# Kernel optimization log

Hardware: AMD Instinct MI355X
Metric: run time of the kernel (lower is better)

The kernel has to match this reference:

```python
import jax, jax.numpy as jnp
import numpy as np

B, S, D, QD, OUT = 32, 2048, 768, 256, 1024

def setup_inputs() -> dict:
    key = jax.random.key(0)
    k = jax.random.split(key, 8)
    data = jax.random.normal(k[0], (B, S, D), dtype=jnp.float32)
    seq_len = jax.random.randint(k[1], (B,), 0, S)
    # learned params (Linear: y = x @ W.T + b)
    s1 = 1.0 / np.sqrt(D)
    s3 = 1.0 / np.sqrt(QD)
    W1 = jax.random.uniform(k[2], (QD, D), minval=-s1, maxval=s1, dtype=jnp.float32)
    b1 = jax.random.uniform(k[3], (QD,), minval=-s1, maxval=s1, dtype=jnp.float32)
    W2 = jax.random.uniform(k[4], (QD, D), minval=-s1, maxval=s1, dtype=jnp.float32)
    b2 = jax.random.uniform(k[5], (QD,), minval=-s1, maxval=s1, dtype=jnp.float32)
    W3 = jax.random.uniform(k[6], (OUT, QD), minval=-s3, maxval=s3, dtype=jnp.float32)
    b3 = jax.random.uniform(k[7], (OUT,), minval=-s3, maxval=s3, dtype=jnp.float32)
    return {"data": data, "seq_len": seq_len, "W1": W1, "b1": b1,
            "W2": W2, "b2": b2, "W3": W3, "b3": b3}

def reference(data, seq_len, W1, b1, W2, b2, W3, b3):
    # Q, K projections: [B,S,QD]
    Q = jnp.einsum('bsd,qd->bsq', data, W1) + b1
    K = jnp.einsum('bsd,qd->bsq', data, W2) + b2
    # scores = K @ Q^T / sqrt(QD): [B,S,S]
    scores = jnp.einsum('biq,bjq->bij', K, Q) / np.sqrt(QD).astype(np.float32)
    attn = jax.nn.softmax(scores, axis=2)
    # attention output uses K as values: [B,S,QD]
    x = jnp.einsum('bij,bjq->biq', attn, K)
    # max-pool over sequence dim -> [B,QD]
    x = jnp.max(x, axis=1)
    out = jax.nn.relu(jnp.einsum('bq,oq->bo', x, W3) + b3)
    return out
```

## Files before the change

kernel.cpp:

```cpp
#include <hip/hip_runtime.h>
#include <hip/hip_bf16.h>

#define Bn   32
#define Sn   2048
#define Dn   768
#define QDn  256
#define OUTn 1024

typedef __attribute__((ext_vector_type(8))) short          bf16x8;
typedef __attribute__((ext_vector_type(4))) float          f32x4;
typedef __attribute__((ext_vector_type(8))) unsigned short u16x8;
typedef __attribute__((ext_vector_type(4))) unsigned short u16x4;

typedef unsigned short ushort_t;

__device__ __forceinline__ unsigned short f2bf(float f) {
    unsigned int u = __float_as_uint(f);
    u = (u + 0x7FFFu + ((u >> 16) & 1u)) >> 16;
    return (unsigned short)u;
}
#define MFMA16(a,b,c) __builtin_amdgcn_mfma_f32_16x16x32_bf16((a),(b),(c),0,0,0)

__global__ __launch_bounds__(256) void wconv_kernel(
    const float* __restrict__ W1, const float* __restrict__ W2,
    ushort_t* __restrict__ W1h, ushort_t* __restrict__ W2h)
{
    const int idx = blockIdx.x * 256 + threadIdx.x;
    W1h[idx] = f2bf(W1[idx]);
    W2h[idx] = f2bf(W2[idx]);
}

__global__ __launch_bounds__(256, 2) void proj_kernel(
    const float* __restrict__ data,
    const ushort_t* __restrict__ W1h, const float* __restrict__ b1,
    const ushort_t* __restrict__ W2h, const float* __restrict__ b2,
    ushort_t* __restrict__ Qb, ushort_t* __restrict__ Kb,
    ushort_t* __restrict__ KTb)
{
    __shared__ __align__(16) char smem[34816];
    ushort_t* DH = (ushort_t*)smem;
    ushort_t* WH = (ushort_t*)(smem + 10240);
    ushort_t* EP = (ushort_t*)smem;

    const int tid  = threadIdx.x;
    const int w    = tid >> 6;
    const int quad = (tid >> 4) & 3;
    const int n15  = tid & 15;
    const int mtile = blockIdx.y;
    const int half  = blockIdx.x;
    const bool isQ  = (half == 0);
    const ushort_t* WhP = isQ ? W1h : W2h;
    const float* bp = isQ ? b1 : b2;

    f32x4 acc[2][16];
    #pragma unroll
    for (int i = 0; i < 2; ++i)
        #pragma unroll
        for (int j = 0; j < 16; ++j) acc[i][j] = (f32x4)0.f;

    const size_t drow = (size_t)mtile * 128;

    for (int kt = 0; kt < 24; ++kt) {
        const int kc = kt * 32;
        {
            const int m  = tid >> 1;
            const int k0 = (tid & 1) << 4;
            const float* src = data + (drow + m) * 768 + kc + k0;
            const float4 v0 = *(const float4*)(src);
            const float4 v1 = *(const float4*)(src + 4);
            const float4 v2 = *(const float4*)(src + 8);
            const float4 v3 = *(const float4*)(src + 12);
            u16x8 h0, h1;
            h0[0]=f2bf(v0.x); h0[1]=f2bf(v0.y); h0[2]=f2bf(v0.z); h0[3]=f2bf(v0.w);
            h0[4]=f2bf(v1.x); h0[5]=f2bf(v1.y); h0[6]=f2bf(v1.z); h0[7]=f2bf(v1.w);
            h1[0]=f2bf(v2.x); h1[1]=f2bf(v2.y); h1[2]=f2bf(v2.z); h1[3]=f2bf(v2.w);
            h1[4]=f2bf(v3.x); h1[5]=f2bf(v3.y); h1[6]=f2bf(v3.z); h1[7]=f2bf(v3.w);
            *(u16x8*)&DH[m*40 + k0]     = h0;
            *(u16x8*)&DH[m*40 + k0 + 8] = h1;
        }
        #pragma unroll
        for (int u = 0; u < 4; ++u) {
            const int nrow = (tid >> 2) + u * 64;
            const int ko   = (tid & 3) << 3;
            *(u16x8*)&WH[nrow*40 + ko] = *(const u16x8*)(WhP + (size_t)nrow * 768 + kc + ko);
        }
        __syncthreads();
        bf16x8 ah[2];
        #pragma unroll
        for (int ms = 0; ms < 2; ++ms)
            ah[ms] = *(bf16x8*)&DH[(w*32 + ms*16 + n15)*40 + quad*8];
        #pragma unroll
        for (int ns = 0; ns < 16; ++ns) {
            const bf16x8 bh = *(bf16x8*)&WH[(ns*16 + n15)*40 + quad*8];
            #pragma unroll
            for (int ms = 0; ms < 2; ++ms)
                acc[ms][ns] = MFMA16(ah[ms], bh, acc[ms][ns]);
        }
        __syncthreads();
    }

    float bv[16];
    #pragma unroll
    for (int ns = 0; ns < 16; ++ns) bv[ns] = bp[ns*16 + n15];

    {
        ushort_t* dstRM = isQ ? Qb : Kb;
        #pragma unroll
        for (int hf = 0; hf < 2; ++hf) {
            __syncthreads();
            if ((w >> 1) == hf) {
                #pragma unroll
                for (int ms = 0; ms < 2; ++ms)
                    #pragma unroll
                    for (int ns = 0; ns < 16; ++ns)
                        #pragma unroll
                        for (int r = 0; r < 4; ++r) {
                            const int rl = (w & 1)*32 + ms*16 + quad*4 + r;
                            EP[rl*264 + ns*16 + n15] = f2bf(acc[ms][ns][r] + bv[ns]);
                        }
            }
            __syncthreads();
            const int row = tid >> 2;
            #pragma unroll
            for (int u = 0; u < 8; ++u) {
                const int co = (tid & 3)*8 + u*32;
                *(u16x8*)(dstRM + (drow + hf*64 + row)*256 + co) =
                    *(u16x8*)&EP[row*264 + co];
            }
        }
    }
    if (!isQ) {
        const int bidx = mtile >> 4;
        const int s0   = (mtile & 15) * 128;
        #pragma unroll
        for (int qh = 0; qh < 2; ++qh) {
            __syncthreads();
            #pragma unroll
            for (int ms = 0; ms < 2; ++ms)
                #pragma unroll
                for (int ns8 = 0; ns8 < 8; ++ns8) {
                    const int ns = qh*8 + ns8;
                    #pragma unroll
                    for (int r = 0; r < 4; ++r) {
                        const int rowm = w*32 + ms*16 + quad*4 + r;
                        EP[(ns8*16 + n15)*136 + rowm] = f2bf(acc[ms][ns][r] + bv[ns]);
                    }
                }
            __syncthreads();
            const int q = tid >> 1;
            #pragma unroll
            for (int u = 0; u < 8; ++u) {
                const int mo = (tid & 1)*8 + u*16;
                *(u16x8*)(KTb + ((size_t)(bidx*256 + qh*128 + q))*2048 + s0 + mo) =
                    *(u16x8*)&EP[q*136 + mo];
            }
        }
    }
}

__global__ __launch_bounds__(256, 2) void attn_kernel(
    const ushort_t* __restrict__ Qb, const ushort_t* __restrict__ Kb,
    const ushort_t* __restrict__ KTb, float* __restrict__ pmax)
{
    __shared__ __align__(16) char smem[49664];
    ushort_t* QS = (ushort_t*)smem;
    ushort_t* PS = (ushort_t*)(smem + 32768);
    float*    l_lds = (float*)(smem + 49152);

    const int tid  = threadIdx.x;
    const int w    = tid >> 6;
    const int quad = (tid >> 4) & 3;
    const int n15  = tid & 15;
    const int b    = blockIdx.x;
    const int it   = blockIdx.y;
    const int i0   = it * 128;

    const ushort_t* QbB  = Qb  + (size_t)b * Sn * QDn;
    const ushort_t* KbB  = Kb  + (size_t)b * Sn * QDn;
    const ushort_t* KTbB = KTb + (size_t)b * QDn * Sn;

    bf16x8 kf[2][8];
    #pragma unroll
    for (int isub = 0; isub < 2; ++isub) {
        const size_t irow = (size_t)(i0 + w*32 + isub*16 + n15) * QDn;
        #pragma unroll
        for (int ks = 0; ks < 8; ++ks)
            kf[isub][ks] = *(const bf16x8*)(KbB + irow + ks*32 + quad*8);
    }

    f32x4 xq[4][8];
    #pragma unroll
    for (int qs = 0; qs < 4; ++qs)
        #pragma unroll
        for (int is = 0; is < 8; ++is) xq[qs][is] = (f32x4)0.f;
    float l_i[2] = {0.f, 0.f};

    const int swz  = (n15 & 7) * 8;
    const int jrow = tid >> 2;
    const int wsw  = (jrow & 7) * 8;

    for (int jt = 0; jt < Sn; jt += 64) {
        __syncthreads();
        {
            const ushort_t* src = QbB + (size_t)(jt + jrow) * QDn + (tid & 3) * 64;
            ushort_t* dst = QS + jrow * 256;
            #pragma unroll
            for (int u = 0; u < 8; ++u) {
                const int col = (tid & 3) * 64 + u * 8;
                *(u16x8*)&dst[col ^ wsw] = *(const u16x8*)(src + u * 8);
            }
        }
        __syncthreads();
        f32x4 sc[4][2];
        #pragma unroll
        for (int js = 0; js < 4; ++js) { sc[js][0] = (f32x4)0.f; sc[js][1] = (f32x4)0.f; }
        #pragma unroll
        for (int ks = 0; ks < 8; ++ks) {
            #pragma unroll
            for (int js = 0; js < 4; ++js) {
                const bf16x8 ah = *(bf16x8*)&QS[(js*16 + n15)*256 + ((ks*32 + quad*8) ^ swz)];
                sc[js][0] = MFMA16(ah, kf[0][ks], sc[js][0]);
                sc[js][1] = MFMA16(ah, kf[1][ks], sc[js][1]);
            }
        }
        #pragma unroll
        for (int isub = 0; isub < 2; ++isub) {
            const int prow = (w*32 + isub*16 + n15) * 64;
            float rs = 0.f;
            #pragma unroll
            for (int js = 0; js < 4; ++js) {
                u16x4 ph;
                #pragma unroll
                for (int r = 0; r < 4; ++r) {
                    const float p = __expf(sc[js][isub][r] * 0.0625f);
                    rs += p;
                    ph[r] = f2bf(p);
                }
                *(u16x4*)&PS[prow + ((js*16 + quad*4) ^ swz)] = ph;
            }
            rs += __shfl_xor(rs, 16, 64);
            rs += __shfl_xor(rs, 32, 64);
            l_i[isub] += rs;
        }
        bf16x8 at2[2][4];
        #pragma unroll
        for (int ks2 = 0; ks2 < 2; ++ks2)
            #pragma unroll
            for (int qs = 0; qs < 4; ++qs)
                at2[ks2][qs] = *(const bf16x8*)(
                    KTbB + (size_t)(w*64 + qs*16 + n15) * Sn + jt + ks2*32 + quad*8);
        __syncthreads();
        #pragma unroll
        for (int ks2 = 0; ks2 < 2; ++ks2) {
            #pragma unroll
            for (int is = 0; is < 8; ++is) {
                const bf16x8 pb = *(bf16x8*)&PS[(is*16 + n15)*64 + ((ks2*32 + quad*8) ^ swz)];
                #pragma unroll
                for (int qs = 0; qs < 4; ++qs)
                    xq[qs][is] = MFMA16(at2[ks2][qs], pb, xq[qs][is]);
            }
        }
    }

    __syncthreads();
    if (quad == 0) {
        l_lds[w*32 + n15]      = l_i[0];
        l_lds[w*32 + 16 + n15] = l_i[1];
    }
    __syncthreads();
    float linv[8];
    #pragma unroll
    for (int is = 0; is < 8; ++is) linv[is] = 1.0f / l_lds[is*16 + n15];
    #pragma unroll
    for (int qs = 0; qs < 4; ++qs) {
        #pragma unroll
        for (int r = 0; r < 4; ++r) {
            float mv = xq[qs][0][r] * linv[0];
            #pragma unroll
            for (int is = 1; is < 8; ++is)
                mv = fmaxf(mv, xq[qs][is][r] * linv[is]);
            mv = fmaxf(mv, __shfl_xor(mv, 1, 64));
            mv = fmaxf(mv, __shfl_xor(mv, 2, 64));
            mv = fmaxf(mv, __shfl_xor(mv, 4, 64));
            mv = fmaxf(mv, __shfl_xor(mv, 8, 64));
            if (n15 == 0) {
                const int q = w*64 + qs*16 + quad*4 + r;
                pmax[((size_t)b * 16 + it) * QDn + q] = mv;
            }
        }
    }
}

__global__ __launch_bounds__(256) void head_kernel(
    const float* __restrict__ pmax,
    const float* __restrict__ W3, const float* __restrict__ b3,
    float* __restrict__ out)
{
    __shared__ float xs[QDn];
    const int b = blockIdx.x, tid = threadIdx.x;
    float m = pmax[((size_t)b * 16) * QDn + tid];
    #pragma unroll
    for (int t = 1; t < 16; ++t)
        m = fmaxf(m, pmax[((size_t)b * 16 + t) * QDn + tid]);
    xs[tid] = m;
    __syncthreads();
    #pragma unroll
    for (int u = 0; u < 4; ++u) {
        const int o = (u << 8) + tid;
        const float4* wv = (const float4*)(W3 + (size_t)o * QDn);
        float s = 0.f;
        #pragma unroll 8
        for (int q4 = 0; q4 < QDn / 4; ++q4) {
            const float4 w4 = wv[q4];
            const float4 x4 = *(const float4*)&xs[q4 << 2];
            s += w4.x * x4.x + w4.y * x4.y + w4.z * x4.z + w4.w * x4.w;
        }
        out[(size_t)b * OUTn + o] = fmaxf(s + b3[o], 0.f);
    }
}

extern "C" void kernel_launch(void* const* d_in, const int* in_sizes, int n_in,
                              void* d_out, int out_size, void* d_ws, size_t ws_size,
                              hipStream_t stream) {
    const float* data = (const float*)d_in[0];
    const float* W1 = (const float*)d_in[2];
    const float* b1 = (const float*)d_in[3];
    const float* W2 = (const float*)d_in[4];
    const float* b2 = (const float*)d_in[5];
    const float* W3 = (const float*)d_in[6];
    const float* b3 = (const float*)d_in[7];
    float* out = (float*)d_out;

    ushort_t* Qb  = (ushort_t*)d_ws;
    ushort_t* Kb  = Qb  + 16777216;
    ushort_t* KTb = Kb  + 16777216;
    float*    pmax = (float*)((char*)d_ws + 100663296);
    ushort_t* W1h = (ushort_t*)((char*)d_ws + 100663296 + 524288);
    ushort_t* W2h = W1h + 196608;

    wconv_kernel<<<768, 256, 0, stream>>>(W1, W2, W1h, W2h);
    dim3 gP(2, 512);
    proj_kernel<<<gP, 256, 0, stream>>>(data, W1h, b1, W2h, b2, Qb, Kb, KTb);
    dim3 gA(Bn, 16);
    attn_kernel<<<gA, 256, 0, stream>>>(Qb, Kb, KTb, pmax);
    head_kernel<<<Bn, 256, 0, stream>>>(pmax, W3, b3, out);
}
```

Baseline: 663.9 us.

## Async global-to-LDS Q loads, pre-convert data to bf16, split head kernel

The attention kernel now stages each Q tile into LDS with global_load_lds instructions issued for the next tile while the current PV MFMAs run. This replaces the synchronous register round-trip and drops one barrier per iteration. The KT loads are also issued earlier. When the workspace is large enough, a separate kernel converts data to bf16 first so the projection kernel reads half the bytes, at the cost of an extra pass over the input. The head kernel is split across four blocks per batch to add parallelism.

```diff
diff --git a/kernel.cpp b/kernel.cpp
--- a/kernel.cpp
+++ b/kernel.cpp
@@ -21,6 +21,13 @@
 }
 #define MFMA16(a,b,c) __builtin_amdgcn_mfma_f32_16x16x32_bf16((a),(b),(c),0,0,0)
 
+__device__ __forceinline__ void gll16(const ushort_t* g, ushort_t* l) {
+    __builtin_amdgcn_global_load_lds(
+        (const __attribute__((address_space(1))) unsigned int*)g,
+        (__attribute__((address_space(3))) unsigned int*)l,
+        16, 0, 0);
+}
+
 __global__ __launch_bounds__(256) void wconv_kernel(
     const float* __restrict__ W1, const float* __restrict__ W2,
     ushort_t* __restrict__ W1h, ushort_t* __restrict__ W2h)
@@ -30,8 +37,21 @@
     W2h[idx] = f2bf(W2[idx]);
 }
 
+__global__ __launch_bounds__(256) void dconv_kernel(
+    const float* __restrict__ in, ushort_t* __restrict__ outb)
+{
+    const size_t i8 = ((size_t)blockIdx.x * 256 + threadIdx.x) * 8;
+    const float4 a = *(const float4*)(in + i8);
+    const float4 b = *(const float4*)(in + i8 + 4);
+    u16x8 h;
+    h[0]=f2bf(a.x); h[1]=f2bf(a.y); h[2]=f2bf(a.z); h[3]=f2bf(a.w);
+    h[4]=f2bf(b.x); h[5]=f2bf(b.y); h[6]=f2bf(b.z); h[7]=f2bf(b.w);
+    *(u16x8*)(outb + i8) = h;
+}
+
+template<bool USE_DB>
 __global__ __launch_bounds__(256, 2) void proj_kernel(
-    const float* __restrict__ data,
+    const float* __restrict__ data, const ushort_t* __restrict__ Db,
     const ushort_t* __restrict__ W1h, const float* __restrict__ b1,
     const ushort_t* __restrict__ W2h, const float* __restrict__ b2,
     ushort_t* __restrict__ Qb, ushort_t* __restrict__ Kb,
@@ -62,7 +82,13 @@
 
     for (int kt = 0; kt < 24; ++kt) {
         const int kc = kt * 32;
-        {
+        if (USE_DB) {
+            const int m  = tid >> 1;
+            const int k0 = (tid & 1) << 4;
+            const ushort_t* src = Db + (drow + m) * 768 + kc + k0;
+            *(u16x8*)&DH[m*40 + k0]     = *(const u16x8*)(src);
+            *(u16x8*)&DH[m*40 + k0 + 8] = *(const u16x8*)(src + 8);
+        } else {
             const int m  = tid >> 1;
             const int k0 = (tid & 1) << 4;
             const float* src = data + (drow + m) * 768 + kc + k0;
@@ -169,6 +195,7 @@
 
     const int tid  = threadIdx.x;
     const int w    = tid >> 6;
+    const int lane = tid & 63;
     const int quad = (tid >> 4) & 3;
     const int n15  = tid & 15;
     const int b    = blockIdx.x;
@@ -179,6 +206,22 @@
     const ushort_t* KbB  = Kb  + (size_t)b * Sn * QDn;
     const ushort_t* KTbB = KTb + (size_t)b * QDn * Sn;
 
+    const int grow_l = (lane >> 5);
+    const int gcol   = (lane & 31) * 8;
+
+    f32x4 xq[4][8];
+    #pragma unroll
+    for (int qs = 0; qs < 4; ++qs)
+        #pragma unroll
+        for (int is = 0; is < 8; ++is) xq[qs][is] = (f32x4)0.f;
+    float l_i[2] = {0.f, 0.f};
+
+    #pragma unroll
+    for (int i = 0; i < 8; ++i) {
+        const int row = w*16 + i*2 + grow_l;
+        const int csw = gcol ^ ((row & 7) << 3);
+        gll16(QbB + (size_t)row * QDn + csw, QS + (w*16 + i*2) * 256);
+    }
     bf16x8 kf[2][8];
     #pragma unroll
     for (int isub = 0; isub < 2; ++isub) {
@@ -187,30 +230,11 @@
         for (int ks = 0; ks < 8; ++ks)
             kf[isub][ks] = *(const bf16x8*)(KbB + irow + ks*32 + quad*8);
     }
-
-    f32x4 xq[4][8];
-    #pragma unroll
-    for (int qs = 0; qs < 4; ++qs)
-        #pragma unroll
-        for (int is = 0; is < 8; ++is) xq[qs][is] = (f32x4)0.f;
-    float l_i[2] = {0.f, 0.f};
-
-    const int swz  = (n15 & 7) * 8;
-    const int jrow = tid >> 2;
-    const int wsw  = (jrow & 7) * 8;
+    __syncthreads();
+
+    const int swz = (n15 & 7) * 8;
 
     for (int jt = 0; jt < Sn; jt += 64) {
-        __syncthreads();
-        {
-            const ushort_t* src = QbB + (size_t)(jt + jrow) * QDn + (tid & 3) * 64;
-            ushort_t* dst = QS + jrow * 256;
-            #pragma unroll
-            for (int u = 0; u < 8; ++u) {
-                const int col = (tid & 3) * 64 + u * 8;
-                *(u16x8*)&dst[col ^ wsw] = *(const u16x8*)(src + u * 8);
-            }
-        }
-        __syncthreads();
         f32x4 sc[4][2];
         #pragma unroll
         for (int js = 0; js < 4; ++js) { sc[js][0] = (f32x4)0.f; sc[js][1] = (f32x4)0.f; }
@@ -223,6 +247,7 @@
                 sc[js][1] = MFMA16(ah, kf[1][ks], sc[js][1]);
             }
         }
+        bf16x8 at2[2][4];
         #pragma unroll
         for (int isub = 0; isub < 2; ++isub) {
             const int prow = (w*32 + isub*16 + n15) * 64;
@@ -241,15 +266,24 @@
             rs += __shfl_xor(rs, 16, 64);
             rs += __shfl_xor(rs, 32, 64);
             l_i[isub] += rs;
-        }
-        bf16x8 at2[2][4];
-        #pragma unroll
-        for (int ks2 = 0; ks2 < 2; ++ks2)
-            #pragma unroll
-            for (int qs = 0; qs < 4; ++qs)
-                at2[ks2][qs] = *(const bf16x8*)(
-                    KTbB + (size_t)(w*64 + qs*16 + n15) * Sn + jt + ks2*32 + quad*8);
+            if (isub == 0) {
+                #pragma unroll
+                for (int ks2 = 0; ks2 < 2; ++ks2)
+                    #pragma unroll
+                    for (int qs = 0; qs < 4; ++qs)
+                        at2[ks2][qs] = *(const bf16x8*)(
+                            KTbB + (size_t)(w*64 + qs*16 + n15) * Sn + jt + ks2*32 + quad*8);
+            }
+        }
         __syncthreads();
+        if (jt + 64 < Sn) {
+            #pragma unroll
+            for (int i = 0; i < 8; ++i) {
+                const int row = w*16 + i*2 + grow_l;
+                const int csw = gcol ^ ((row & 7) << 3);
+                gll16(QbB + (size_t)(jt + 64 + row) * QDn + csw, QS + (w*16 + i*2) * 256);
+            }
+        }
         #pragma unroll
         for (int ks2 = 0; ks2 < 2; ++ks2) {
             #pragma unroll
@@ -260,9 +294,9 @@
                     xq[qs][is] = MFMA16(at2[ks2][qs], pb, xq[qs][is]);
             }
         }
-    }
-
-    __syncthreads();
+        __syncthreads();
+    }
+
     if (quad == 0) {
         l_lds[w*32 + n15]      = l_i[0];
         l_lds[w*32 + 16 + n15] = l_i[1];
@@ -304,19 +338,16 @@
         m = fmaxf(m, pmax[((size_t)b * 16 + t) * QDn + tid]);
     xs[tid] = m;
     __syncthreads();
-    #pragma unroll
-    for (int u = 0; u < 4; ++u) {
-        const int o = (u << 8) + tid;
-        const float4* wv = (const float4*)(W3 + (size_t)o * QDn);
-        float s = 0.f;
-        #pragma unroll 8
-        for (int q4 = 0; q4 < QDn / 4; ++q4) {
-            const float4 w4 = wv[q4];
-            const float4 x4 = *(const float4*)&xs[q4 << 2];
-            s += w4.x * x4.x + w4.y * x4.y + w4.z * x4.z + w4.w * x4.w;
-        }
-        out[(size_t)b * OUTn + o] = fmaxf(s + b3[o], 0.f);
-    }
+    const int o = blockIdx.y * 256 + tid;
+    const float4* wv = (const float4*)(W3 + (size_t)o * QDn);
+    float s = 0.f;
+    #pragma unroll 8
+    for (int q4 = 0; q4 < QDn / 4; ++q4) {
+        const float4 w4 = wv[q4];
+        const float4 x4 = *(const float4*)&xs[q4 << 2];
+        s += w4.x * x4.x + w4.y * x4.y + w4.z * x4.z + w4.w * x4.w;
+    }
+    out[(size_t)b * OUTn + o] = fmaxf(s + b3[o], 0.f);
 }
 
 extern "C" void kernel_launch(void* const* d_in, const int* in_sizes, int n_in,
@@ -337,11 +368,19 @@
     float*    pmax = (float*)((char*)d_ws + 100663296);
     ushort_t* W1h = (ushort_t*)((char*)d_ws + 100663296 + 524288);
     ushort_t* W2h = W1h + 196608;
+    ushort_t* Db  = (ushort_t*)((char*)d_ws + 101974016);
+    const bool useDb = (ws_size >= 202637312ull);
 
     wconv_kernel<<<768, 256, 0, stream>>>(W1, W2, W1h, W2h);
     dim3 gP(2, 512);
-    proj_kernel<<<gP, 256, 0, stream>>>(data, W1h, b1, W2h, b2, Qb, Kb, KTb);
+    if (useDb) {
+        dconv_kernel<<<24576, 256, 0, stream>>>(data, Db);
+        proj_kernel<true><<<gP, 256, 0, stream>>>(data, Db, W1h, b1, W2h, b2, Qb, Kb, KTb);
+    } else {
+        proj_kernel<false><<<gP, 256, 0, stream>>>(data, Db, W1h, b1, W2h, b2, Qb, Kb, KTb);
+    }
     dim3 gA(Bn, 16);
     attn_kernel<<<gA, 256, 0, stream>>>(Qb, Kb, KTb, pmax);
-    head_kernel<<<Bn, 256, 0, stream>>>(pmax, W3, b3, out);
-}
+    dim3 gH(Bn, 4);
+    head_kernel<<<gH, 256, 0, stream>>>(pmax, W3, b3, out);
+}
```

Measured after the change: 882.9 us. 33.0% more time.
